# Kernel optimization log

Measured on AMD Instinct MI355X. Metric: run time of the kernel, lower is better.

The kernel has to match this reference:

```python
import jax, jax.numpy as jnp
import numpy as np

S_DIM, I_DIM, O_DIM = 1024, 2048, 1024
TOTAL = S_DIM + I_DIM + O_DIM  # 4096
INPUT_DIM, NUM_CLASSES, BATCH = 2048, 1000, 256


def setup_inputs() -> dict:
    key = jax.random.key(0)
    ks = jax.random.split(key, 6)
    x = jax.random.normal(ks[0], (BATCH, INPUT_DIM), dtype=jnp.float32)
    W = jax.random.normal(ks[1], (TOTAL, TOTAL), dtype=jnp.float32) * 0.02
    # torch Linear: weight [out, in], bias [out]
    in_w = jax.random.normal(ks[2], (S_DIM, INPUT_DIM), dtype=jnp.float32) * (1.0 / np.sqrt(INPUT_DIM))
    in_b = jax.random.normal(ks[3], (S_DIM,), dtype=jnp.float32) * 0.01
    out_w = jax.random.normal(ks[4], (NUM_CLASSES, O_DIM), dtype=jnp.float32) * (1.0 / np.sqrt(O_DIM))
    out_b = jax.random.normal(ks[5], (NUM_CLASSES,), dtype=jnp.float32) * 0.01
    return {"x": x, "W": W, "in_w": in_w, "in_b": in_b, "out_w": out_w, "out_b": out_b, "time_steps": 10}


def reference(x, W, in_w, in_b, out_w, out_b, time_steps):
    B = x.shape[0]
    S, I, O = S_DIM, I_DIM, O_DIM
    # slice effective W into 9 sub-blocks (use_lora=False -> W_eff = W)
    W_ss, W_sr, W_so = W[:S, :S], W[:S, S:S + I], W[:S, S + I:]
    W_rs, W_rr, W_ro = W[S:S + I, :S], W[S:S + I, S:S + I], W[S:S + I, S + I:]
    W_os, W_or, W_oo = W[S + I:, :S], W[S + I:, S:S + I], W[S + I:, S + I:]

    E = x @ in_w.T + in_b  # [B, S]
    gate = (jnp.arange(time_steps) % 5 == 0).astype(x.dtype)  # E injected when t%5==0

    init = (jnp.zeros((B, S), x.dtype), jnp.zeros((B, I), x.dtype), jnp.zeros((B, O), x.dtype))

    def step(carry, g):
        Ss, Is, Os = carry
        S_next = jax.nn.relu(Ss @ W_ss + g * E + Is @ W_rs + Os @ W_os)
        I_next = jax.nn.relu(Is @ W_rr + Ss @ W_sr + Os @ W_or)
        O_next = jax.nn.relu(Os @ W_oo + Is @ W_ro + Ss @ W_so)
        return (S_next, I_next, O_next), None

    (Ss, Is, Os), _ = jax.lax.scan(step, init, gate)
    return Os @ out_w.T + out_b  # [B, num_classes]
```

## Files before the change

### kernel.cpp

```cpp
#include <hip/hip_runtime.h>


typedef __bf16 bf16x8 __attribute__((ext_vector_type(8)));
typedef float  f32x16 __attribute__((ext_vector_type(16)));

#define TOTAL 4096
#define BATCH 256
#define INDIM 2048
#define SDIM  1024
#define NCLS  1000

#define MFMA(a, b, c) __builtin_amdgcn_mfma_f32_32x32x16_bf16((a), (b), (c), 0, 0, 0)

__device__ inline f32x16 zero16() {
    f32x16 v;
#pragma unroll
    for (int i = 0; i < 16; ++i) v[i] = 0.f;
    return v;
}

__device__ inline void swz_slot(const float* __restrict__ in, __bf16* __restrict__ out,
                                int C, int Rvalid, int t) {
    const int lane = t & 63;
    const int frag = t >> 6;
    const int kcN = C >> 4;
    const int rt = frag / kcN;
    const int kc = frag - rt * kcN;
    const int r = rt * 32 + (lane & 31);
    const int c = kc * 16 + (lane >> 5) * 8;
    alignas(16) __bf16 v[8];
    if (r < Rvalid) {
        const float* p = in + (size_t)r * C + c;
#pragma unroll
        for (int j = 0; j < 8; ++j) v[j] = (__bf16)p[j];
    } else {
#pragma unroll
        for (int j = 0; j < 8; ++j) v[j] = (__bf16)0.f;
    }
    *(ulonglong2*)(out + (size_t)t * 8) = *(const ulonglong2*)v;
}

__global__ __launch_bounds__(256) void k_prep(const float* __restrict__ W,
                                              const float* __restrict__ x,
                                              const float* __restrict__ in_w,
                                              const float* __restrict__ in_b,
                                              const float* __restrict__ out_w,
                                              __bf16* __restrict__ WT,
                                              __bf16* __restrict__ OWT,
                                              float* __restrict__ Ebuf,
                                              __bf16* __restrict__ H0) {
    __shared__ float t[16 * 512];
    const int bid = blockIdx.x;
    const int tid = threadIdx.x;
    if (bid < 256) {
        float* red = t;
        const int mt = bid >> 5, nt = bid & 31;
        const int wave = tid >> 6, lane = tid & 63;
        const int l31 = lane & 31, kh = (lane >> 5) * 8;
        const int k0 = wave * 512;
        const float* Ax = x    + (size_t)(mt * 32 + l31) * INDIM + k0 + kh;
        const float* Bw = in_w + (size_t)(nt * 32 + l31) * INDIM + k0 + kh;
        f32x16 acc = zero16();
#pragma unroll 4
        for (int i = 0; i < 32; ++i) {
            const float* pa = Ax + i * 16;
            const float* pb = Bw + i * 16;
            float4 a0 = *(const float4*)pa, a1 = *(const float4*)(pa + 4);
            float4 b0 = *(const float4*)pb, b1 = *(const float4*)(pb + 4);
            bf16x8 a, b;
            a[0] = (__bf16)a0.x; a[1] = (__bf16)a0.y; a[2] = (__bf16)a0.z; a[3] = (__bf16)a0.w;
            a[4] = (__bf16)a1.x; a[5] = (__bf16)a1.y; a[6] = (__bf16)a1.z; a[7] = (__bf16)a1.w;
            b[0] = (__bf16)b0.x; b[1] = (__bf16)b0.y; b[2] = (__bf16)b0.z; b[3] = (__bf16)b0.w;
            b[4] = (__bf16)b1.x; b[5] = (__bf16)b1.y; b[6] = (__bf16)b1.z; b[7] = (__bf16)b1.w;
            acc = MFMA(a, b, acc);
        }
#pragma unroll
        for (int r = 0; r < 16; ++r) {
            int row = (r & 3) + 8 * (r >> 2) + 4 * (lane >> 5);
            red[wave * 1024 + row * 32 + l31] = acc[r];
        }
        __syncthreads();
        const int e0 = tid * 4;
        float4 s = {0.f, 0.f, 0.f, 0.f};
#pragma unroll
        for (int w = 0; w < 4; ++w) {
            float4 v = *(const float4*)&red[w * 1024 + e0];
            s.x += v.x; s.y += v.y; s.z += v.z; s.w += v.w;
        }
        const int row = e0 >> 5, col = e0 & 31;
        const int m = mt * 32 + row, n = nt * 32 + col;
        float v[4] = {s.x + in_b[n], s.y + in_b[n + 1], s.z + in_b[n + 2], s.w + in_b[n + 3]};
        *(float4*)(Ebuf + m * SDIM + n) = *(const float4*)v;
        alignas(8) __bf16 o[4];
#pragma unroll
        for (int j = 0; j < 4; ++j) o[j] = (__bf16)fmaxf(v[j], 0.f);
        const size_t frag = (size_t)(m >> 5) * (TOTAL / 16) + (n >> 4);
        const int lh = (m & 31) + 32 * ((n >> 3) & 1);
        *(ushort4*)(H0 + frag * 512 + lh * 8 + (n & 7)) = *(const ushort4*)o;
    } else if (bid < 2304) {
        const int wb = bid - 256;
        const int k0 = (wb >> 3) * 16;
        const int n0 = (wb & 7) * 512;
#pragma unroll
        for (int i = 0; i < 8; ++i) {
            const int slot = i * 256 + tid;
            const int row = slot >> 7;
            const int c4 = (slot & 127) * 4;
            float4 v = *(const float4*)(W + (size_t)(k0 + row) * TOTAL + n0 + c4);
            *(float4*)&t[row * 512 + c4] = v;
        }
        __syncthreads();
        const int kcG = k0 >> 4;
#pragma unroll
        for (int s = tid; s < 1024; s += 256) {
            const int rtl = s >> 6;
            const int lane = s & 63;
            const int nl = rtl * 32 + (lane & 31);
            const int kl = (lane >> 5) * 8;
            bf16x8 v;
#pragma unroll
            for (int j = 0; j < 8; ++j) v[j] = (__bf16)t[(kl + j) * 512 + nl];
            const size_t fragG = (size_t)((n0 >> 5) + rtl) * (TOTAL / 16) + kcG;
            *(bf16x8*)(WT + fragG * 512 + lane * 8) = v;
        }
    } else {
        swz_slot(out_w, OWT, 1024, NCLS, (bid - 2304) * 256 + tid);
    }
}

template <int CHUNKS>
__global__ __launch_bounds__(512, 2) void k_step(const __bf16* __restrict__ h,
                                                 const __bf16* __restrict__ WT,
                                                 const float* __restrict__ E,
                                                 const int gate,
                                                 __bf16* __restrict__ hn) {
    __shared__ float buf[4][4096];
    const int wave = threadIdx.x >> 6;
    const int lane = threadIdx.x & 63;
    const int xcd = blockIdx.x & 7;
    const int idx = blockIdx.x >> 3;
    const int mt = idx & 3;
    const int nt = xcd * 8 + (idx >> 2);
    constexpr int PER = CHUNKS >> 3;
    const int kc0 = wave * PER;

    const bf16x8* A0 = (const bf16x8*)h  + ((size_t)(mt * 2) * (TOTAL / 16) + kc0) * 64 + lane;
    const bf16x8* A1 = A0 + (size_t)(TOTAL / 16) * 64;
    const bf16x8* B0 = (const bf16x8*)WT + ((size_t)(nt * 2) * (TOTAL / 16) + kc0) * 64 + lane;
    const bf16x8* B1 = B0 + (size_t)(TOTAL / 16) * 64;

    f32x16 ac0 = zero16(), ac1 = zero16(), ac2 = zero16(), ac3 = zero16();
#pragma unroll 4
    for (int i = 0; i < PER; ++i) {
        const int off = i * 64;
        bf16x8 a0 = A0[off];
        bf16x8 a1 = A1[off];
        bf16x8 b0 = B0[off];
        bf16x8 b1 = B1[off];
        ac0 = MFMA(a0, b0, ac0);
        ac1 = MFMA(a0, b1, ac1);
        ac2 = MFMA(a1, b0, ac2);
        ac3 = MFMA(a1, b1, ac3);
    }

    f32x16 accs[4] = {ac0, ac1, ac2, ac3};
    if (wave >= 4) {
        float* b = buf[wave - 4];
#pragma unroll
        for (int c = 0; c < 4; ++c)
#pragma unroll
            for (int r = 0; r < 16; ++r)
                b[(c * 16 + r) * 64 + lane] = accs[c][r];
    }
    __syncthreads();
    if (wave < 4) {
        float* b = buf[wave];
#pragma unroll
        for (int c = 0; c < 4; ++c)
#pragma unroll
            for (int r = 0; r < 16; ++r) {
                const int i2 = (c * 16 + r) * 64 + lane;
                b[i2] += accs[c][r];
            }
    }
    __syncthreads();

    const int t = threadIdx.x;
    const int c = t >> 7;
    const int r = (t >> 3) & 15;
    const int l0 = (t & 7) * 8;
    const int base = (c * 16 + r) * 64 + l0;
    float4 s0 = {0.f, 0.f, 0.f, 0.f}, s1 = {0.f, 0.f, 0.f, 0.f};
#pragma unroll
    for (int w = 0; w < 4; ++w) {
        const float4* p = (const float4*)&buf[w][base];
        float4 v0 = p[0], v1 = p[1];
        s0.x += v0.x; s0.y += v0.y; s0.z += v0.z; s0.w += v0.w;
        s1.x += v1.x; s1.y += v1.y; s1.z += v1.z; s1.w += v1.w;
    }
    float v[8] = {s0.x, s0.y, s0.z, s0.w, s1.x, s1.y, s1.z, s1.w};
    const int ih = c >> 1, jh = c & 1;
    const int row = ih * 32 + (r & 3) + 8 * (r >> 2) + 4 * (l0 >> 5);
    const int col0 = jh * 32 + (l0 & 31);
    const int m = mt * 64 + row;
    const int n0g = nt * 64 + col0;
    if (gate && n0g < SDIM) {
        const float* Ep = E + m * SDIM + n0g;
#pragma unroll
        for (int j = 0; j < 8; ++j) v[j] += Ep[j];
    }
    alignas(16) __bf16 o[8];
#pragma unroll
    for (int j = 0; j < 8; ++j) o[j] = (__bf16)fmaxf(v[j], 0.f);
    const size_t frag = (size_t)(m >> 5) * (TOTAL / 16) + (n0g >> 4);
    const int lh = (m & 31) + 32 * ((n0g >> 3) & 1);
    *(ulonglong2*)(hn + frag * 512 + lh * 8) = *(const ulonglong2*)o;
}

__global__ __launch_bounds__(512, 4) void k_out(const __bf16* __restrict__ h,
                                                const __bf16* __restrict__ owt,
                                                const float* __restrict__ out_b,
                                                float* __restrict__ out) {
    __shared__ float red[8][1024];
    const int wave = threadIdx.x >> 6;
    const int lane = threadIdx.x & 63;
    const int mt = blockIdx.x >> 5;
    const int ct = blockIdx.x & 31;
    const int m0 = mt * 32, c0 = ct * 32;
    const int kcA0 = (3072 / 16) + wave * 8;
    const int kcB0 = wave * 8;
    const bf16x8* Ap = (const bf16x8*)h   + ((size_t)mt * (TOTAL / 16) + kcA0) * 64 + lane;
    const bf16x8* Bp = (const bf16x8*)owt + ((size_t)ct * (1024 / 16) + kcB0) * 64 + lane;
    f32x16 acc = zero16();
#pragma unroll
    for (int i = 0; i < 8; ++i)
        acc = MFMA(Ap[i * 64], Bp[i * 64], acc);
#pragma unroll
    for (int r = 0; r < 16; ++r) {
        int row = (r & 3) + 8 * (r >> 2) + 4 * (lane >> 5);
        red[wave][row * 32 + (lane & 31)] = acc[r];
    }
    __syncthreads();
    const int e0 = threadIdx.x * 2;
    float sx = 0.f, sy = 0.f;
#pragma unroll
    for (int w = 0; w < 8; ++w) {
        float2 v = *(const float2*)&red[w][e0];
        sx += v.x; sy += v.y;
    }
    const int row = e0 >> 5, col = e0 & 31;
    const int m = m0 + row;
    const int n = c0 + col;
    if (n < NCLS)     out[m * NCLS + n]     = sx + out_b[n];
    if (n + 1 < NCLS) out[m * NCLS + n + 1] = sy + out_b[n + 1];
}

extern "C" void kernel_launch(void* const* d_in, const int* in_sizes, int n_in,
                              void* d_out, int out_size, void* d_ws, size_t ws_size,
                              hipStream_t stream) {
    const float* x     = (const float*)d_in[0];
    const float* W     = (const float*)d_in[1];
    const float* in_w  = (const float*)d_in[2];
    const float* in_b  = (const float*)d_in[3];
    const float* out_w = (const float*)d_in[4];
    const float* out_b = (const float*)d_in[5];
    float* out = (float*)d_out;

    char* ws = (char*)d_ws;
    __bf16* WT  = (__bf16*)(ws + 0);
    __bf16* OWT = (__bf16*)(ws + 33554432);
    float*  Ebuf= (float*)(ws + 35651584);
    __bf16* H0  = (__bf16*)(ws + 36700160);
    __bf16* H1  = (__bf16*)(ws + 38797312);

    k_prep<<<2816, 256, 0, stream>>>(W, x, in_w, in_b, out_w, WT, OWT, Ebuf, H0);

    const __bf16* hs = H0;
    __bf16* hd = H1;
    for (int t = 1; t < 10; ++t) {
        const int gate = (t % 5 == 0) ? 1 : 0;
        if (t == 1)
            k_step<SDIM / 16><<<256, 512, 0, stream>>>(hs, WT, Ebuf, gate, hd);
        else
            k_step<TOTAL / 16><<<256, 512, 0, stream>>>(hs, WT, Ebuf, gate, hd);
        const __bf16* tmp = hs; hs = hd; hd = (__bf16*)tmp;
    }

    k_out<<<256, 512, 0, stream>>>(hs, OWT, out_b, out);
}
```

Measured before the change: 263.4 us.

## Fuse recurrent steps into persistent cooperative kernel and split-K the final step

Replaces the eight separate per-step launches (t=1..8) with one cooperative persistent kernel that loops over time steps with grid-wide syncs, removing launch gaps and tail effects. The last step is reduced to only the output-state columns, since only O is consumed by the readout, and those columns are computed with split-K across 256 blocks plus a small reduction kernel to recover parallelism. This adds grid.sync overhead, a dependence on cooperative launch residency, and an extra fp32 partial buffer round trip.

```diff
diff --git a/kernel.cpp b/kernel.cpp
--- a/kernel.cpp
+++ b/kernel.cpp
@@ -1,4 +1,7 @@
 #include <hip/hip_runtime.h>
+#include <hip/hip_cooperative_groups.h>
+
+namespace cg = cooperative_groups;
 
 
 typedef __bf16 bf16x8 __attribute__((ext_vector_type(8)));
@@ -128,12 +131,11 @@
     }
 }
 
-template <int CHUNKS>
-__global__ __launch_bounds__(512, 2) void k_step(const __bf16* __restrict__ h,
-                                                 const __bf16* __restrict__ WT,
-                                                 const float* __restrict__ E,
-                                                 const int gate,
-                                                 __bf16* __restrict__ hn) {
+__global__ __launch_bounds__(512, 2) void k_steps(const __bf16* __restrict__ WT,
+                                                  const float* __restrict__ E,
+                                                  __bf16* __restrict__ H0,
+                                                  __bf16* __restrict__ H1) {
+    cg::grid_group grid = cg::this_grid();
     __shared__ float buf[4][4096];
     const int wave = threadIdx.x >> 6;
     const int lane = threadIdx.x & 63;
@@ -141,8 +143,106 @@
     const int idx = blockIdx.x >> 3;
     const int mt = idx & 3;
     const int nt = xcd * 8 + (idx >> 2);
-    constexpr int PER = CHUNKS >> 3;
-    const int kc0 = wave * PER;
+
+    const int tt = threadIdx.x;
+    const int c = tt >> 7;
+    const int r = (tt >> 3) & 15;
+    const int l0 = (tt & 7) * 8;
+    const int base = (c * 16 + r) * 64 + l0;
+    const int ih = c >> 1, jh = c & 1;
+    const int row = ih * 32 + (r & 3) + 8 * (r >> 2) + 4 * (l0 >> 5);
+    const int col0 = jh * 32 + (l0 & 31);
+    const int m = mt * 64 + row;
+    const int n0g = nt * 64 + col0;
+
+    const __bf16* hs = H0;
+    __bf16* hd = H1;
+
+    for (int t = 1; t <= 8; ++t) {
+        const int per = (t == 1) ? 8 : 32;
+        const int kc0 = wave * per;
+        const bf16x8* A0 = (const bf16x8*)hs + ((size_t)(mt * 2) * (TOTAL / 16) + kc0) * 64 + lane;
+        const bf16x8* A1 = A0 + (size_t)(TOTAL / 16) * 64;
+        const bf16x8* B0 = (const bf16x8*)WT + ((size_t)(nt * 2) * (TOTAL / 16) + kc0) * 64 + lane;
+        const bf16x8* B1 = B0 + (size_t)(TOTAL / 16) * 64;
+
+        f32x16 ac0 = zero16(), ac1 = zero16(), ac2 = zero16(), ac3 = zero16();
+#pragma unroll 4
+        for (int i = 0; i < per; ++i) {
+            const int off = i * 64;
+            bf16x8 a0 = A0[off];
+            bf16x8 a1 = A1[off];
+            bf16x8 b0 = B0[off];
+            bf16x8 b1 = B1[off];
+            ac0 = MFMA(a0, b0, ac0);
+            ac1 = MFMA(a0, b1, ac1);
+            ac2 = MFMA(a1, b0, ac2);
+            ac3 = MFMA(a1, b1, ac3);
+        }
+
+        f32x16 accs[4] = {ac0, ac1, ac2, ac3};
+        if (wave >= 4) {
+            float* b = buf[wave - 4];
+#pragma unroll
+            for (int cc = 0; cc < 4; ++cc)
+#pragma unroll
+                for (int rr = 0; rr < 16; ++rr)
+                    b[(cc * 16 + rr) * 64 + lane] = accs[cc][rr];
+        }
+        __syncthreads();
+        if (wave < 4) {
+            float* b = buf[wave];
+#pragma unroll
+            for (int cc = 0; cc < 4; ++cc)
+#pragma unroll
+                for (int rr = 0; rr < 16; ++rr) {
+                    const int i2 = (cc * 16 + rr) * 64 + lane;
+                    b[i2] += accs[cc][rr];
+                }
+        }
+        __syncthreads();
+
+        float4 s0 = {0.f, 0.f, 0.f, 0.f}, s1 = {0.f, 0.f, 0.f, 0.f};
+#pragma unroll
+        for (int w = 0; w < 4; ++w) {
+            const float4* p = (const float4*)&buf[w][base];
+            float4 v0 = p[0], v1 = p[1];
+            s0.x += v0.x; s0.y += v0.y; s0.z += v0.z; s0.w += v0.w;
+            s1.x += v1.x; s1.y += v1.y; s1.z += v1.z; s1.w += v1.w;
+        }
+        float v[8] = {s0.x, s0.y, s0.z, s0.w, s1.x, s1.y, s1.z, s1.w};
+        if (t == 5 && n0g < SDIM) {
+            const float* Ep = E + m * SDIM + n0g;
+#pragma unroll
+            for (int j = 0; j < 8; ++j) v[j] += Ep[j];
+        }
+        alignas(16) __bf16 o[8];
+#pragma unroll
+        for (int j = 0; j < 8; ++j) o[j] = (__bf16)fmaxf(v[j], 0.f);
+        const size_t frag = (size_t)(m >> 5) * (TOTAL / 16) + (n0g >> 4);
+        const int lh = (m & 31) + 32 * ((n0g >> 3) & 1);
+        *(ulonglong2*)(hd + frag * 512 + lh * 8) = *(const ulonglong2*)o;
+
+        if (t < 8) {
+            __threadfence();
+            grid.sync();
+        }
+        const __bf16* tmp = hs; hs = hd; hd = (__bf16*)tmp;
+    }
+}
+
+__global__ __launch_bounds__(512, 2) void k_part9(const __bf16* __restrict__ h,
+                                                  const __bf16* __restrict__ WT,
+                                                  float* __restrict__ P) {
+    __shared__ float buf[4][4096];
+    const int wave = threadIdx.x >> 6;
+    const int lane = threadIdx.x & 63;
+    const int xcd = blockIdx.x & 7;
+    const int idx = blockIdx.x >> 3;
+    const int nt = 48 + xcd * 2 + (idx >> 4);
+    const int mt = (idx >> 2) & 3;
+    const int ks = idx & 3;
+    const int kc0 = ks * 64 + wave * 8;
 
     const bf16x8* A0 = (const bf16x8*)h  + ((size_t)(mt * 2) * (TOTAL / 16) + kc0) * 64 + lane;
     const bf16x8* A1 = A0 + (size_t)(TOTAL / 16) * 64;
@@ -151,7 +251,7 @@
 
     f32x16 ac0 = zero16(), ac1 = zero16(), ac2 = zero16(), ac3 = zero16();
 #pragma unroll 4
-    for (int i = 0; i < PER; ++i) {
+    for (int i = 0; i < 8; ++i) {
         const int off = i * 64;
         bf16x8 a0 = A0[off];
         bf16x8 a1 = A1[off];
@@ -198,20 +298,37 @@
         s0.x += v0.x; s0.y += v0.y; s0.z += v0.z; s0.w += v0.w;
         s1.x += v1.x; s1.y += v1.y; s1.z += v1.z; s1.w += v1.w;
     }
-    float v[8] = {s0.x, s0.y, s0.z, s0.w, s1.x, s1.y, s1.z, s1.w};
+    alignas(16) float v[8] = {s0.x, s0.y, s0.z, s0.w, s1.x, s1.y, s1.z, s1.w};
     const int ih = c >> 1, jh = c & 1;
     const int row = ih * 32 + (r & 3) + 8 * (r >> 2) + 4 * (l0 >> 5);
     const int col0 = jh * 32 + (l0 & 31);
     const int m = mt * 64 + row;
-    const int n0g = nt * 64 + col0;
-    if (gate && n0g < SDIM) {
-        const float* Ep = E + m * SDIM + n0g;
-#pragma unroll
-        for (int j = 0; j < 8; ++j) v[j] += Ep[j];
+    const int nl = (nt - 48) * 64 + col0;
+    float* p = P + ((size_t)ks << 18) + (size_t)m * 1024 + nl;
+    *(float4*)p = *(const float4*)&v[0];
+    *(float4*)(p + 4) = *(const float4*)&v[4];
+}
+
+__global__ __launch_bounds__(256) void k_red9(const float* __restrict__ P,
+                                              __bf16* __restrict__ hn) {
+    const int g = blockIdx.x * 256 + threadIdx.x;
+    const int m = g >> 7;
+    const int n8 = (g & 127) << 3;
+    const float* p = P + (size_t)m * 1024 + n8;
+    float4 a0 = *(const float4*)p, a1 = *(const float4*)(p + 4);
+#pragma unroll
+    for (int ks = 1; ks < 4; ++ks) {
+        const float* q = p + ((size_t)ks << 18);
+        float4 b0 = *(const float4*)q, b1 = *(const float4*)(q + 4);
+        a0.x += b0.x; a0.y += b0.y; a0.z += b0.z; a0.w += b0.w;
+        a1.x += b1.x; a1.y += b1.y; a1.z += b1.z; a1.w += b1.w;
     }
     alignas(16) __bf16 o[8];
-#pragma unroll
-    for (int j = 0; j < 8; ++j) o[j] = (__bf16)fmaxf(v[j], 0.f);
+    o[0] = (__bf16)fmaxf(a0.x, 0.f); o[1] = (__bf16)fmaxf(a0.y, 0.f);
+    o[2] = (__bf16)fmaxf(a0.z, 0.f); o[3] = (__bf16)fmaxf(a0.w, 0.f);
+    o[4] = (__bf16)fmaxf(a1.x, 0.f); o[5] = (__bf16)fmaxf(a1.y, 0.f);
+    o[6] = (__bf16)fmaxf(a1.z, 0.f); o[7] = (__bf16)fmaxf(a1.w, 0.f);
+    const int n0g = 3072 + n8;
     const size_t frag = (size_t)(m >> 5) * (TOTAL / 16) + (n0g >> 4);
     const int lh = (m & 31) + 32 * ((n0g >> 3) & 1);
     *(ulonglong2*)(hn + frag * 512 + lh * 8) = *(const ulonglong2*)o;
@@ -272,19 +389,21 @@
     float*  Ebuf= (float*)(ws + 35651584);
     __bf16* H0  = (__bf16*)(ws + 36700160);
     __bf16* H1  = (__bf16*)(ws + 38797312);
+    float*  Pbuf= (float*)(ws + 40894464);
 
     k_prep<<<2816, 256, 0, stream>>>(W, x, in_w, in_b, out_w, WT, OWT, Ebuf, H0);
 
-    const __bf16* hs = H0;
-    __bf16* hd = H1;
-    for (int t = 1; t < 10; ++t) {
-        const int gate = (t % 5 == 0) ? 1 : 0;
-        if (t == 1)
-            k_step<SDIM / 16><<<256, 512, 0, stream>>>(hs, WT, Ebuf, gate, hd);
-        else
-            k_step<TOTAL / 16><<<256, 512, 0, stream>>>(hs, WT, Ebuf, gate, hd);
-        const __bf16* tmp = hs; hs = hd; hd = (__bf16*)tmp;
-    }
-
-    k_out<<<256, 512, 0, stream>>>(hs, OWT, out_b, out);
-}
+    {
+        const __bf16* wt = WT;
+        const float* eb = Ebuf;
+        __bf16* h0 = H0;
+        __bf16* h1 = H1;
+        void* args[] = {(void*)&wt, (void*)&eb, (void*)&h0, (void*)&h1};
+        hipLaunchCooperativeKernel((void*)k_steps, dim3(256), dim3(512), args, 0, stream);
+    }
+
+    k_part9<<<256, 512, 0, stream>>>(H0, WT, Pbuf);
+    k_red9<<<128, 256, 0, stream>>>(Pbuf, H1);
+
+    k_out<<<256, 512, 0, stream>>>(H1, OWT, out_b, out);
+}
```

New measurement: 821.3 us. +211.7%, slower.
